# Kernel optimization log

Measured on AMD Instinct MI355X. Metric: run time of the kernel, lower is better.

## Reference

```python
import jax, jax.numpy as jnp
import numpy as np

EMB = 1024
HEAD = 64  # emb_size // head_nb = 1024 // 16

def setup_inputs() -> dict:
    key = jax.random.key(0)
    kx, kq, kk, kv = jax.random.split(key, 4)
    x = jax.random.normal(kx, (8, 2048, EMB), dtype=jnp.float32)
    # torch nn.Linear(EMB, HEAD) weight has shape [HEAD, EMB]; y = x @ W.T
    s = 1.0 / np.sqrt(EMB)
    Wq = jax.random.uniform(kq, (HEAD, EMB), jnp.float32, -s, s)
    Wk = jax.random.uniform(kk, (HEAD, EMB), jnp.float32, -s, s)
    Wv = jax.random.uniform(kv, (HEAD, EMB), jnp.float32, -s, s)
    return {"x": x, "Wq": Wq, "Wk": Wk, "Wv": Wv}

def reference(x, Wq, Wk, Wv):
    B, T, C = x.shape
    q = jnp.einsum('btc,hc->bth', x, Wq)  # [B,T,H]
    k = jnp.einsum('btc,hc->bth', x, Wk)
    v = jnp.einsum('btc,hc->bth', x, Wv)
    scale = 1.0 / jnp.sqrt(jnp.float32(q.shape[-1]))
    wei = jnp.einsum('bth,bsh->bts', q, k) * scale  # [B,T,T]
    causal = jnp.tril(jnp.ones((T, T), dtype=bool))
    wei = jnp.where(causal, wei, -jnp.inf)
    wei = jax.nn.softmax(wei, axis=-1)
    # dropout is identity in eval mode
    out = jnp.einsum('bts,bsh->bth', wei, v)  # [B,T,H]
    return out
```

## Files before the change

### kernel.cpp

```cpp
#include <hip/hip_runtime.h>
#include <math.h>

#define SEQ  2048
#define NROW 16384
#define HEAD 64
#define EMB  1024

typedef __attribute__((ext_vector_type(8))) short short8;
typedef __attribute__((ext_vector_type(4))) float f32x4;

static __device__ __forceinline__ unsigned short f2bf(float f) {
    unsigned u = __builtin_bit_cast(unsigned, f);
    u += 0x7fffu + ((u >> 16) & 1u);
    return (unsigned short)(u >> 16);
}
static __device__ __forceinline__ float bf2f(unsigned short u) {
    unsigned v = (unsigned)u << 16;
    return __builtin_bit_cast(float, v);
}
static __device__ __forceinline__ ushort4 cvt4(float4 f) {
    ushort4 u;
    u.x = f2bf(f.x); u.y = f2bf(f.y); u.z = f2bf(f.z); u.w = f2bf(f.w);
    return u;
}

static __device__ __forceinline__ void gload_lds16(const void* g, void* l) {
    __builtin_amdgcn_global_load_lds(
        (const __attribute__((address_space(1))) unsigned int*)g,
        (__attribute__((address_space(3))) unsigned int*)l, 16, 0, 0);
}

__global__ __launch_bounds__(256) void wcvt_kernel(
    const float* __restrict__ Wq, const float* __restrict__ Wk,
    const float* __restrict__ Wv, unsigned short* __restrict__ Wb)
{
    const int idx = (blockIdx.x * 256 + threadIdx.x) * 4;
    const int h = idx >> 10;
    const float* src;
    if (h < 64)       src = Wq + idx;
    else if (h < 128) src = Wk + (idx - 65536);
    else              src = Wv + (idx - 131072);
    *(ushort4*)(Wb + idx) = cvt4(*(const float4*)src);
}

__global__ __launch_bounds__(512, 2) void qkv_mfma_kernel(
    const float* __restrict__ x, const unsigned short* __restrict__ Wb,
    unsigned short* __restrict__ qN, unsigned short* __restrict__ kN,
    unsigned short* __restrict__ vT)
{
    __shared__ unsigned short As[2][64][72];
    __shared__ unsigned short Bs[2][192 * 64];

    const int tid  = threadIdx.x;
    const int w    = tid >> 6;
    const int lane = tid & 63;
    const int col  = lane & 15;
    const int quad = lane >> 4;
    const int row0 = blockIdx.x * 64;
    const int wm   = w >> 2;
    const int wn   = w & 3;
    const int pq   = (quad ^ (col & 7)) * 8;

    const int ar_r = tid >> 4, ar_c = tid & 15;
    const float* xg = x + (size_t)(row0 + ar_r) * EMB + ar_c * 4;

    const int sr = lane >> 3, cc = (lane & 7) ^ sr;
    const unsigned short* bg = Wb;

    {
        float4 fa[2];
#pragma unroll
        for (int j = 0; j < 2; ++j) fa[j] = *(const float4*)(xg + (size_t)(32 * j) * EMB);
#pragma unroll
        for (int j = 0; j < 2; ++j) *(ushort4*)&As[0][ar_r + 32 * j][ar_c * 4] = cvt4(fa[j]);
#pragma unroll
        for (int j = 0; j < 3; ++j) {
            const int c = w * 3 + j;
            gload_lds16(bg + (size_t)(c * 8 + sr) * EMB + cc * 8,
                        &Bs[0][c * 8 * 64]);
        }
    }
    __syncthreads();

    f32x4 acc[2][3];
#pragma unroll
    for (int mf = 0; mf < 2; ++mf)
#pragma unroll
        for (int t = 0; t < 3; ++t) acc[mf][t] = (f32x4){0.f, 0.f, 0.f, 0.f};

    float4 fa[2];
#pragma unroll 2
    for (int kt = 0; kt < 16; ++kt) {
        const int cur = kt & 1;
        if (kt + 1 < 16) {
            const int k0 = (kt + 1) * 64;
#pragma unroll
            for (int j = 0; j < 3; ++j) {
                const int c = w * 3 + j;
                gload_lds16(bg + (size_t)(c * 8 + sr) * EMB + k0 + cc * 8,
                            &Bs[cur ^ 1][c * 8 * 64]);
            }
#pragma unroll
            for (int j = 0; j < 2; ++j)
                fa[j] = *(const float4*)(xg + (size_t)(32 * j) * EMB + k0);
        }
#pragma unroll
        for (int ks = 0; ks < 2; ++ks) {
            short8 af0 = *(const short8*)&As[cur][wm * 32 + col][ks * 32 + quad * 8];
            short8 af1 = *(const short8*)&As[cur][wm * 32 + 16 + col][ks * 32 + quad * 8];
            const int po = pq ^ (ks * 32);
#pragma unroll
            for (int t = 0; t < 3; ++t) {
                short8 bf = *(const short8*)
                    &Bs[cur][(wn * 48 + t * 16 + col) * 64 + po];
                acc[0][t] = __builtin_amdgcn_mfma_f32_16x16x32_bf16(af0, bf, acc[0][t], 0, 0, 0);
                acc[1][t] = __builtin_amdgcn_mfma_f32_16x16x32_bf16(af1, bf, acc[1][t], 0, 0, 0);
            }
        }
        if (kt + 1 < 16) {
#pragma unroll
            for (int j = 0; j < 2; ++j)
                *(ushort4*)&As[cur ^ 1][ar_r + 32 * j][ar_c * 4] = cvt4(fa[j]);
        }
        __syncthreads();
    }

#pragma unroll
    for (int mf = 0; mf < 2; ++mf) {
        const int ro = row0 + wm * 32 + mf * 16 + quad * 4;
#pragma unroll
        for (int t = 0; t < 3; ++t) {
            const int hb = wn * 48 + 16 * t;
            const int h  = hb + col;
            if (hb < 64) {
#pragma unroll
                for (int r = 0; r < 4; ++r)
                    qN[(size_t)(ro + r) * HEAD + h] = f2bf(acc[mf][t][r] * 0.125f);
            } else if (hb < 128) {
#pragma unroll
                for (int r = 0; r < 4; ++r)
                    kN[(size_t)(ro + r) * HEAD + (h - 64)] = f2bf(acc[mf][t][r]);
            } else {
                ushort4 uv;
                uv.x = f2bf(acc[mf][t][0]); uv.y = f2bf(acc[mf][t][1]);
                uv.z = f2bf(acc[mf][t][2]); uv.w = f2bf(acc[mf][t][3]);
                *(ushort4*)(vT + (size_t)(h - 128) * NROW + ro) = uv;
            }
        }
    }
}

__global__ __launch_bounds__(512, 2) void attn_kernel(
    const unsigned short* __restrict__ qN,
    const unsigned short* __restrict__ kN,
    const unsigned short* __restrict__ vT,
    unsigned short* __restrict__ op,
    float2* __restrict__ ml)
{
    __shared__ unsigned short Ks[2][64 * 64];
    __shared__ unsigned short Vs[2][64 * 64];
    __shared__ unsigned short Pl[8][32][72];

    const int qt   = 7 - (int)blockIdx.x;
    const int b    = blockIdx.y;
    const int p    = blockIdx.z;
    const int tid  = threadIdx.x;
    const int wv   = tid >> 6;
    const int lane = tid & 63;
    const int col  = lane & 15;
    const int quad = lane >> 4;

    const int q0   = qt * 256 + wv * 16;
    const int q0g  = b * SEQ + q0;
    const int Cb   = 4 * qt + 4;
    const int kt0  = (Cb * p) >> 2;
    const int kt1  = (Cb * (p + 1)) >> 2;
    const int ktp  = min(kt0, Cb - 1);

    const int sr = lane >> 3, cc = (lane & 7) ^ sr;
    const int pq = (quad ^ (col & 7)) * 8;
    const unsigned short* kgb = kN + (size_t)(b * SEQ) * HEAD;
    const int bcol = b * SEQ;

    const short8* qp0 = (const short8*)qN + (size_t)(q0g + col) * 8;
    const short8* qp1 = (const short8*)qN + (size_t)(q0g + 128 + col) * 8;
    short8 aq00 = qp0[quad], aq01 = qp0[quad + 4];
    short8 aq10 = qp1[quad], aq11 = qp1[quad + 4];

    f32x4 o[2][4];
    float l_i[2][4];
#pragma unroll
    for (int mi = 0; mi < 2; ++mi)
#pragma unroll
        for (int t = 0; t < 4; ++t) {
            o[mi][t] = (f32x4){0.f, 0.f, 0.f, 0.f};
            l_i[mi][t] = 0.f;
        }

    {
        const int r = wv * 8 + sr;
        gload_lds16(kgb + (size_t)(ktp * 64 + r) * HEAD + cc * 8,
                    &Ks[0][wv * 8 * 64]);
        gload_lds16(vT + (size_t)r * NROW + bcol + ktp * 64 + cc * 8,
                    &Vs[0][wv * 8 * 64]);
    }
    __syncthreads();

    for (int kt = kt0; kt < kt1; ++kt) {
        const int cur = (kt - kt0) & 1;
        const int s0  = kt * 64;
        const bool dz = (kt >= Cb - 4);
        const bool m0 = (kt < Cb - 2);

        if (kt + 1 < kt1) {
            const int r = wv * 8 + sr;
            gload_lds16(kgb + (size_t)((kt + 1) * 64 + r) * HEAD + cc * 8,
                        &Ks[cur ^ 1][wv * 8 * 64]);
            gload_lds16(vT + (size_t)r * NROW + bcol + (kt + 1) * 64 + cc * 8,
                        &Vs[cur ^ 1][wv * 8 * 64]);
        }

        f32x4 sv[2][4];
#pragma unroll
        for (int t = 0; t < 4; ++t) {
            sv[0][t] = (f32x4){0.f, 0.f, 0.f, 0.f};
            sv[1][t] = (f32x4){0.f, 0.f, 0.f, 0.f};
        }
#pragma unroll
        for (int t = 0; t < 4; ++t) {
            const int rb = (16 * t + col) * 64;
            short8 kf0 = *(const short8*)&Ks[cur][rb + pq];
            short8 kf1 = *(const short8*)&Ks[cur][rb + (pq ^ 32)];
            sv[1][t] = __builtin_amdgcn_mfma_f32_16x16x32_bf16(aq10, kf0, sv[1][t], 0, 0, 0);
            sv[1][t] = __builtin_amdgcn_mfma_f32_16x16x32_bf16(aq11, kf1, sv[1][t], 0, 0, 0);
            if (m0) {
                sv[0][t] = __builtin_amdgcn_mfma_f32_16x16x32_bf16(aq00, kf0, sv[0][t], 0, 0, 0);
                sv[0][t] = __builtin_amdgcn_mfma_f32_16x16x32_bf16(aq01, kf1, sv[0][t], 0, 0, 0);
            }
        }

#pragma unroll
        for (int mi = 0; mi < 2; ++mi) {
            if (mi == 0 && !m0) continue;
#pragma unroll
            for (int r = 0; r < 4; ++r) {
                const int grow = q0 + mi * 128 + quad * 4 + r;
                float ls = 0.f;
#pragma unroll
                for (int t = 0; t < 4; ++t) {
                    float e = __expf(sv[mi][t][r]);
                    if (dz && (s0 + 16 * t + col > grow)) e = 0.0f;
                    Pl[wv][mi * 16 + quad * 4 + r][16 * t + col] = f2bf(e);
                    ls += e;
                }
                l_i[mi][r] += ls;
            }
        }

        short8 pf00, pf01;
        if (m0) {
            pf00 = *(const short8*)&Pl[wv][col][quad * 8];
            pf01 = *(const short8*)&Pl[wv][col][quad * 8 + 32];
        }
        short8 pf10 = *(const short8*)&Pl[wv][16 + col][quad * 8];
        short8 pf11 = *(const short8*)&Pl[wv][16 + col][quad * 8 + 32];

#pragma unroll
        for (int tn = 0; tn < 4; ++tn) {
            const int rb = (16 * tn + col) * 64;
            short8 vf0 = *(const short8*)&Vs[cur][rb + pq];
            short8 vf1 = *(const short8*)&Vs[cur][rb + (pq ^ 32)];
            o[1][tn] = __builtin_amdgcn_mfma_f32_16x16x32_bf16(pf10, vf0, o[1][tn], 0, 0, 0);
            o[1][tn] = __builtin_amdgcn_mfma_f32_16x16x32_bf16(pf11, vf1, o[1][tn], 0, 0, 0);
            if (m0) {
                o[0][tn] = __builtin_amdgcn_mfma_f32_16x16x32_bf16(pf00, vf0, o[0][tn], 0, 0, 0);
                o[0][tn] = __builtin_amdgcn_mfma_f32_16x16x32_bf16(pf01, vf1, o[0][tn], 0, 0, 0);
            }
        }

        __syncthreads();
    }

#pragma unroll
    for (int mi = 0; mi < 2; ++mi) {
#pragma unroll
        for (int r = 0; r < 4; ++r) {
            float l = l_i[mi][r];
            l += __shfl_xor(l, 1, 16);
            l += __shfl_xor(l, 2, 16);
            l += __shfl_xor(l, 4, 16);
            l += __shfl_xor(l, 8, 16);
            l_i[mi][r] = l;
        }
        const int ro = q0g + mi * 128 + quad * 4;
#pragma unroll
        for (int tn = 0; tn < 4; ++tn)
#pragma unroll
            for (int r = 0; r < 4; ++r)
                op[((size_t)p * NROW + ro + r) * HEAD + 16 * tn + col] =
                    f2bf(o[mi][tn][r]);
        if (col == 0) {
#pragma unroll
            for (int r = 0; r < 4; ++r)
                ml[p * NROW + ro + r] = make_float2(0.0f, l_i[mi][r]);
        }
    }
}

__global__ __launch_bounds__(256) void merge_kernel(
    const unsigned short* __restrict__ op, const float2* __restrict__ ml,
    float* __restrict__ out)
{
    const int idx = blockIdx.x * 256 + threadIdx.x;
    const int row = idx >> 4;
    const int hc  = (idx & 15) * 4;

    float denom = 0.0f;
#pragma unroll
    for (int p = 0; p < 4; ++p) denom += ml[p * NROW + row].y;
    const float inv = 1.0f / denom;

    float4 r = make_float4(0.f, 0.f, 0.f, 0.f);
#pragma unroll
    for (int p = 0; p < 4; ++p) {
        ushort4 u = *(const ushort4*)(op + ((size_t)p * NROW + row) * HEAD + hc);
        r.x += bf2f(u.x);
        r.y += bf2f(u.y);
        r.z += bf2f(u.z);
        r.w += bf2f(u.w);
    }
    r.x *= inv; r.y *= inv; r.z *= inv; r.w *= inv;
    *(float4*)(out + (size_t)row * HEAD + hc) = r;
}

extern "C" void kernel_launch(void* const* d_in, const int* in_sizes, int n_in,
                              void* d_out, int out_size, void* d_ws, size_t ws_size,
                              hipStream_t stream)
{
    const float* x  = (const float*)d_in[0];
    const float* Wq = (const float*)d_in[1];
    const float* Wk = (const float*)d_in[2];
    const float* Wv = (const float*)d_in[3];

    char* w = (char*)d_ws;
    unsigned short* qN = (unsigned short*)w;
    unsigned short* kN = (unsigned short*)(w + (2u << 20));
    unsigned short* vT = (unsigned short*)(w + (4u << 20));
    unsigned short* Wb = (unsigned short*)(w + (6u << 20));
    unsigned short* op = (unsigned short*)(w + (6u << 20) + 393216);
    float2*         ml = (float2*)(w + (14u << 20) + 393216);
    float* out = (float*)d_out;

    wcvt_kernel<<<192, 256, 0, stream>>>(Wq, Wk, Wv, Wb);
    qkv_mfma_kernel<<<256, 512, 0, stream>>>(x, Wb, qN, kN, vT);
    attn_kernel<<<dim3(8, 8, 4), 512, 0, stream>>>(qN, kN, vT, op, ml);
    merge_kernel<<<1024, 256, 0, stream>>>(op, ml, out);
}
```

Measured before the change: 138.1 us.

## Fuse four kernels into one cooperative kernel with grid-wide syncs

Merges the weight conversion, QKV projection GEMM, causal attention and split merge into one persistent cooperative kernel of 256 blocks. Stages are separated by grid.sync() with thread fences rather than by separate launches. This is meant to remove three kernel-launch gaps and the drain and fill between kernels. In exchange it drops the occupancy hint in launch bounds, depends on all 256 blocks of 512 threads being co-resident, and adds grid barrier cost plus load imbalance in the attention stage.

Measured after the change: 380.4 us. +175.5%, slower.

```diff
diff --git a/kernel.cpp b/kernel.cpp
--- a/kernel.cpp
+++ b/kernel.cpp
@@ -1,5 +1,8 @@
 #include <hip/hip_runtime.h>
+#include <hip/hip_cooperative_groups.h>
 #include <math.h>
+
+namespace cg = cooperative_groups;
 
 #define SEQ  2048
 #define NROW 16384
@@ -30,307 +33,318 @@
         (__attribute__((address_space(3))) unsigned int*)l, 16, 0, 0);
 }
 
-__global__ __launch_bounds__(256) void wcvt_kernel(
-    const float* __restrict__ Wq, const float* __restrict__ Wk,
-    const float* __restrict__ Wv, unsigned short* __restrict__ Wb)
+__global__ __launch_bounds__(512) void fused_kernel(
+    const float* __restrict__ x, const float* __restrict__ Wq,
+    const float* __restrict__ Wk, const float* __restrict__ Wv,
+    unsigned short* __restrict__ Wb, unsigned short* __restrict__ qN,
+    unsigned short* __restrict__ kN, unsigned short* __restrict__ vT,
+    unsigned short* __restrict__ op,
+    float2* __restrict__ ml,
+    float* __restrict__ out)
 {
-    const int idx = (blockIdx.x * 256 + threadIdx.x) * 4;
-    const int h = idx >> 10;
-    const float* src;
-    if (h < 64)       src = Wq + idx;
-    else if (h < 128) src = Wk + (idx - 65536);
-    else              src = Wv + (idx - 131072);
-    *(ushort4*)(Wb + idx) = cvt4(*(const float4*)src);
-}
-
-__global__ __launch_bounds__(512, 2) void qkv_mfma_kernel(
-    const float* __restrict__ x, const unsigned short* __restrict__ Wb,
-    unsigned short* __restrict__ qN, unsigned short* __restrict__ kN,
-    unsigned short* __restrict__ vT)
-{
-    __shared__ unsigned short As[2][64][72];
-    __shared__ unsigned short Bs[2][192 * 64];
-
-    const int tid  = threadIdx.x;
-    const int w    = tid >> 6;
-    const int lane = tid & 63;
-    const int col  = lane & 15;
-    const int quad = lane >> 4;
-    const int row0 = blockIdx.x * 64;
-    const int wm   = w >> 2;
-    const int wn   = w & 3;
-    const int pq   = (quad ^ (col & 7)) * 8;
-
-    const int ar_r = tid >> 4, ar_c = tid & 15;
-    const float* xg = x + (size_t)(row0 + ar_r) * EMB + ar_c * 4;
-
-    const int sr = lane >> 3, cc = (lane & 7) ^ sr;
-    const unsigned short* bg = Wb;
+    __shared__ __align__(16) char smem[69632];
+    cg::grid_group grid = cg::this_grid();
+
+    const int tid = threadIdx.x;
+    const int bid = blockIdx.x;
 
     {
-        float4 fa[2];
-#pragma unroll
-        for (int j = 0; j < 2; ++j) fa[j] = *(const float4*)(xg + (size_t)(32 * j) * EMB);
-#pragma unroll
-        for (int j = 0; j < 2; ++j) *(ushort4*)&As[0][ar_r + 32 * j][ar_c * 4] = cvt4(fa[j]);
-#pragma unroll
-        for (int j = 0; j < 3; ++j) {
-            const int c = w * 3 + j;
-            gload_lds16(bg + (size_t)(c * 8 + sr) * EMB + cc * 8,
-                        &Bs[0][c * 8 * 64]);
+        const int gid = bid * 512 + tid;
+        if (gid < 49152) {
+            const int idx = gid * 4;
+            const int h = idx >> 10;
+            const float* src;
+            if (h < 64)       src = Wq + idx;
+            else if (h < 128) src = Wk + (idx - 65536);
+            else              src = Wv + (idx - 131072);
+            *(ushort4*)(Wb + idx) = cvt4(*(const float4*)src);
         }
     }
-    __syncthreads();
-
-    f32x4 acc[2][3];
-#pragma unroll
-    for (int mf = 0; mf < 2; ++mf)
-#pragma unroll
-        for (int t = 0; t < 3; ++t) acc[mf][t] = (f32x4){0.f, 0.f, 0.f, 0.f};
-
-    float4 fa[2];
-#pragma unroll 2
-    for (int kt = 0; kt < 16; ++kt) {
-        const int cur = kt & 1;
-        if (kt + 1 < 16) {
-            const int k0 = (kt + 1) * 64;
+    __threadfence();
+    grid.sync();
+
+    {
+        unsigned short (*As)[64][72] = (unsigned short (*)[64][72])smem;
+        unsigned short (*Bs)[192 * 64] =
+            (unsigned short (*)[192 * 64])(smem + 18432);
+
+        const int w    = tid >> 6;
+        const int lane = tid & 63;
+        const int col  = lane & 15;
+        const int quad = lane >> 4;
+        const int row0 = bid * 64;
+        const int wm   = w >> 2;
+        const int wn   = w & 3;
+        const int pq   = (quad ^ (col & 7)) * 8;
+
+        const int ar_r = tid >> 4, ar_c = tid & 15;
+        const float* xg = x + (size_t)(row0 + ar_r) * EMB + ar_c * 4;
+
+        const int sr = lane >> 3, cc = (lane & 7) ^ sr;
+        const unsigned short* bg = Wb;
+
+        {
+            float4 fa[2];
+#pragma unroll
+            for (int j = 0; j < 2; ++j) fa[j] = *(const float4*)(xg + (size_t)(32 * j) * EMB);
+#pragma unroll
+            for (int j = 0; j < 2; ++j) *(ushort4*)&As[0][ar_r + 32 * j][ar_c * 4] = cvt4(fa[j]);
 #pragma unroll
             for (int j = 0; j < 3; ++j) {
                 const int c = w * 3 + j;
-                gload_lds16(bg + (size_t)(c * 8 + sr) * EMB + k0 + cc * 8,
-                            &Bs[cur ^ 1][c * 8 * 64]);
-            }
-#pragma unroll
-            for (int j = 0; j < 2; ++j)
-                fa[j] = *(const float4*)(xg + (size_t)(32 * j) * EMB + k0);
-        }
-#pragma unroll
-        for (int ks = 0; ks < 2; ++ks) {
-            short8 af0 = *(const short8*)&As[cur][wm * 32 + col][ks * 32 + quad * 8];
-            short8 af1 = *(const short8*)&As[cur][wm * 32 + 16 + col][ks * 32 + quad * 8];
-            const int po = pq ^ (ks * 32);
+                gload_lds16(bg + (size_t)(c * 8 + sr) * EMB + cc * 8,
+                            &Bs[0][c * 8 * 64]);
+            }
+        }
+        __syncthreads();
+
+        f32x4 acc[2][3];
+#pragma unroll
+        for (int mf = 0; mf < 2; ++mf)
+#pragma unroll
+            for (int t = 0; t < 3; ++t) acc[mf][t] = (f32x4){0.f, 0.f, 0.f, 0.f};
+
+        float4 fa[2];
+#pragma unroll 2
+        for (int kt = 0; kt < 16; ++kt) {
+            const int cur = kt & 1;
+            if (kt + 1 < 16) {
+                const int k0 = (kt + 1) * 64;
+#pragma unroll
+                for (int j = 0; j < 3; ++j) {
+                    const int c = w * 3 + j;
+                    gload_lds16(bg + (size_t)(c * 8 + sr) * EMB + k0 + cc * 8,
+                                &Bs[cur ^ 1][c * 8 * 64]);
+                }
+#pragma unroll
+                for (int j = 0; j < 2; ++j)
+                    fa[j] = *(const float4*)(xg + (size_t)(32 * j) * EMB + k0);
+            }
+#pragma unroll
+            for (int ks = 0; ks < 2; ++ks) {
+                short8 af0 = *(const short8*)&As[cur][wm * 32 + col][ks * 32 + quad * 8];
+                short8 af1 = *(const short8*)&As[cur][wm * 32 + 16 + col][ks * 32 + quad * 8];
+                const int po = pq ^ (ks * 32);
+#pragma unroll
+                for (int t = 0; t < 3; ++t) {
+                    short8 bf = *(const short8*)
+                        &Bs[cur][(wn * 48 + t * 16 + col) * 64 + po];
+                    acc[0][t] = __builtin_amdgcn_mfma_f32_16x16x32_bf16(af0, bf, acc[0][t], 0, 0, 0);
+                    acc[1][t] = __builtin_amdgcn_mfma_f32_16x16x32_bf16(af1, bf, acc[1][t], 0, 0, 0);
+                }
+            }
+            if (kt + 1 < 16) {
+#pragma unroll
+                for (int j = 0; j < 2; ++j)
+                    *(ushort4*)&As[cur ^ 1][ar_r + 32 * j][ar_c * 4] = cvt4(fa[j]);
+            }
+            __syncthreads();
+        }
+
+#pragma unroll
+        for (int mf = 0; mf < 2; ++mf) {
+            const int ro = row0 + wm * 32 + mf * 16 + quad * 4;
 #pragma unroll
             for (int t = 0; t < 3; ++t) {
-                short8 bf = *(const short8*)
-                    &Bs[cur][(wn * 48 + t * 16 + col) * 64 + po];
-                acc[0][t] = __builtin_amdgcn_mfma_f32_16x16x32_bf16(af0, bf, acc[0][t], 0, 0, 0);
-                acc[1][t] = __builtin_amdgcn_mfma_f32_16x16x32_bf16(af1, bf, acc[1][t], 0, 0, 0);
-            }
-        }
-        if (kt + 1 < 16) {
-#pragma unroll
-            for (int j = 0; j < 2; ++j)
-                *(ushort4*)&As[cur ^ 1][ar_r + 32 * j][ar_c * 4] = cvt4(fa[j]);
+                const int hb = wn * 48 + 16 * t;
+                const int h  = hb + col;
+                if (hb < 64) {
+#pragma unroll
+                    for (int r = 0; r < 4; ++r)
+                        qN[(size_t)(ro + r) * HEAD + h] = f2bf(acc[mf][t][r] * 0.125f);
+                } else if (hb < 128) {
+#pragma unroll
+                    for (int r = 0; r < 4; ++r)
+                        kN[(size_t)(ro + r) * HEAD + (h - 64)] = f2bf(acc[mf][t][r]);
+                } else {
+                    ushort4 uv;
+                    uv.x = f2bf(acc[mf][t][0]); uv.y = f2bf(acc[mf][t][1]);
+                    uv.z = f2bf(acc[mf][t][2]); uv.w = f2bf(acc[mf][t][3]);
+                    *(ushort4*)(vT + (size_t)(h - 128) * NROW + ro) = uv;
+                }
+            }
+        }
+    }
+    __threadfence();
+    grid.sync();
+
+    {
+        unsigned short (*Ks)[64 * 64] = (unsigned short (*)[64 * 64])smem;
+        unsigned short (*Vs)[64 * 64] = (unsigned short (*)[64 * 64])(smem + 16384);
+        unsigned short (*Pl)[32][72]  = (unsigned short (*)[32][72])(smem + 32768);
+
+        const int qt   = 7 - (bid & 7);
+        const int b    = (bid >> 3) & 7;
+        const int p    = bid >> 6;
+        const int wv   = tid >> 6;
+        const int lane = tid & 63;
+        const int col  = lane & 15;
+        const int quad = lane >> 4;
+
+        const int q0   = qt * 256 + wv * 16;
+        const int q0g  = b * SEQ + q0;
+        const int Cb   = 4 * qt + 4;
+        const int kt0  = (Cb * p) >> 2;
+        const int kt1  = (Cb * (p + 1)) >> 2;
+        const int ktp  = min(kt0, Cb - 1);
+
+        const int sr = lane >> 3, cc = (lane & 7) ^ sr;
+        const int pq = (quad ^ (col & 7)) * 8;
+        const unsigned short* kgb = kN + (size_t)(b * SEQ) * HEAD;
+        const int bcol = b * SEQ;
+
+        const short8* qp0 = (const short8*)qN + (size_t)(q0g + col) * 8;
+        const short8* qp1 = (const short8*)qN + (size_t)(q0g + 128 + col) * 8;
+        short8 aq00 = qp0[quad], aq01 = qp0[quad + 4];
+        short8 aq10 = qp1[quad], aq11 = qp1[quad + 4];
+
+        f32x4 o[2][4];
+        float l_i[2][4];
+#pragma unroll
+        for (int mi = 0; mi < 2; ++mi)
+#pragma unroll
+            for (int t = 0; t < 4; ++t) {
+                o[mi][t] = (f32x4){0.f, 0.f, 0.f, 0.f};
+                l_i[mi][t] = 0.f;
+            }
+
+        {
+            const int r = wv * 8 + sr;
+            gload_lds16(kgb + (size_t)(ktp * 64 + r) * HEAD + cc * 8,
+                        &Ks[0][wv * 8 * 64]);
+            gload_lds16(vT + (size_t)r * NROW + bcol + ktp * 64 + cc * 8,
+                        &Vs[0][wv * 8 * 64]);
         }
         __syncthreads();
+
+        for (int kt = kt0; kt < kt1; ++kt) {
+            const int cur = (kt - kt0) & 1;
+            const int s0  = kt * 64;
+            const bool dz = (kt >= Cb - 4);
+            const bool m0 = (kt < Cb - 2);
+
+            if (kt + 1 < kt1) {
+                const int r = wv * 8 + sr;
+                gload_lds16(kgb + (size_t)((kt + 1) * 64 + r) * HEAD + cc * 8,
+                            &Ks[cur ^ 1][wv * 8 * 64]);
+                gload_lds16(vT + (size_t)r * NROW + bcol + (kt + 1) * 64 + cc * 8,
+                            &Vs[cur ^ 1][wv * 8 * 64]);
+            }
+
+            f32x4 sv[2][4];
+#pragma unroll
+            for (int t = 0; t < 4; ++t) {
+                sv[0][t] = (f32x4){0.f, 0.f, 0.f, 0.f};
+                sv[1][t] = (f32x4){0.f, 0.f, 0.f, 0.f};
+            }
+#pragma unroll
+            for (int t = 0; t < 4; ++t) {
+                const int rb = (16 * t + col) * 64;
+                short8 kf0 = *(const short8*)&Ks[cur][rb + pq];
+                short8 kf1 = *(const short8*)&Ks[cur][rb + (pq ^ 32)];
+                sv[1][t] = __builtin_amdgcn_mfma_f32_16x16x32_bf16(aq10, kf0, sv[1][t], 0, 0, 0);
+                sv[1][t] = __builtin_amdgcn_mfma_f32_16x16x32_bf16(aq11, kf1, sv[1][t], 0, 0, 0);
+                if (m0) {
+                    sv[0][t] = __builtin_amdgcn_mfma_f32_16x16x32_bf16(aq00, kf0, sv[0][t], 0, 0, 0);
+                    sv[0][t] = __builtin_amdgcn_mfma_f32_16x16x32_bf16(aq01, kf1, sv[0][t], 0, 0, 0);
+                }
+            }
+
+#pragma unroll
+            for (int mi = 0; mi < 2; ++mi) {
+                if (mi == 0 && !m0) continue;
+#pragma unroll
+                for (int r = 0; r < 4; ++r) {
+                    const int grow = q0 + mi * 128 + quad * 4 + r;
+                    float ls = 0.f;
+#pragma unroll
+                    for (int t = 0; t < 4; ++t) {
+                        float e = __expf(sv[mi][t][r]);
+                        if (dz && (s0 + 16 * t + col > grow)) e = 0.0f;
+                        Pl[wv][mi * 16 + quad * 4 + r][16 * t + col] = f2bf(e);
+                        ls += e;
+                    }
+                    l_i[mi][r] += ls;
+                }
+            }
+
+            short8 pf00, pf01;
+            if (m0) {
+                pf00 = *(const short8*)&Pl[wv][col][quad * 8];
+                pf01 = *(const short8*)&Pl[wv][col][quad * 8 + 32];
+            }
+            short8 pf10 = *(const short8*)&Pl[wv][16 + col][quad * 8];
+            short8 pf11 = *(const short8*)&Pl[wv][16 + col][quad * 8 + 32];
+
+#pragma unroll
+            for (int tn = 0; tn < 4; ++tn) {
+                const int rb = (16 * tn + col) * 64;
+                short8 vf0 = *(const short8*)&Vs[cur][rb + pq];
+                short8 vf1 = *(const short8*)&Vs[cur][rb + (pq ^ 32)];
+                o[1][tn] = __builtin_amdgcn_mfma_f32_16x16x32_bf16(pf10, vf0, o[1][tn], 0, 0, 0);
+                o[1][tn] = __builtin_amdgcn_mfma_f32_16x16x32_bf16(pf11, vf1, o[1][tn], 0, 0, 0);
+                if (m0) {
+                    o[0][tn] = __builtin_amdgcn_mfma_f32_16x16x32_bf16(pf00, vf0, o[0][tn], 0, 0, 0);
+                    o[0][tn] = __builtin_amdgcn_mfma_f32_16x16x32_bf16(pf01, vf1, o[0][tn], 0, 0, 0);
+                }
+            }
+
+            __syncthreads();
+        }
+
+#pragma unroll
+        for (int mi = 0; mi < 2; ++mi) {
+#pragma unroll
+            for (int r = 0; r < 4; ++r) {
+                float l = l_i[mi][r];
+                l += __shfl_xor(l, 1, 16);
+                l += __shfl_xor(l, 2, 16);
+                l += __shfl_xor(l, 4, 16);
+                l += __shfl_xor(l, 8, 16);
+                l_i[mi][r] = l;
+            }
+            const int ro = q0g + mi * 128 + quad * 4;
+#pragma unroll
+            for (int tn = 0; tn < 4; ++tn)
+#pragma unroll
+                for (int r = 0; r < 4; ++r)
+                    op[((size_t)p * NROW + ro + r) * HEAD + 16 * tn + col] =
+                        f2bf(o[mi][tn][r]);
+            if (col == 0) {
+#pragma unroll
+                for (int r = 0; r < 4; ++r)
+                    ml[p * NROW + ro + r] = make_float2(0.0f, l_i[mi][r]);
+            }
+        }
     }
-
-#pragma unroll
-    for (int mf = 0; mf < 2; ++mf) {
-        const int ro = row0 + wm * 32 + mf * 16 + quad * 4;
-#pragma unroll
-        for (int t = 0; t < 3; ++t) {
-            const int hb = wn * 48 + 16 * t;
-            const int h  = hb + col;
-            if (hb < 64) {
-#pragma unroll
-                for (int r = 0; r < 4; ++r)
-                    qN[(size_t)(ro + r) * HEAD + h] = f2bf(acc[mf][t][r] * 0.125f);
-            } else if (hb < 128) {
-#pragma unroll
-                for (int r = 0; r < 4; ++r)
-                    kN[(size_t)(ro + r) * HEAD + (h - 64)] = f2bf(acc[mf][t][r]);
-            } else {
-                ushort4 uv;
-                uv.x = f2bf(acc[mf][t][0]); uv.y = f2bf(acc[mf][t][1]);
-                uv.z = f2bf(acc[mf][t][2]); uv.w = f2bf(acc[mf][t][3]);
-                *(ushort4*)(vT + (size_t)(h - 128) * NROW + ro) = uv;
-            }
+    __threadfence();
+    grid.sync();
+
+    {
+#pragma unroll
+        for (int ii = 0; ii < 2; ++ii) {
+            const int idx = ii * 131072 + bid * 512 + tid;
+            const int row = idx >> 4;
+            const int hc  = (idx & 15) * 4;
+
+            float denom = 0.0f;
+#pragma unroll
+            for (int p = 0; p < 4; ++p) denom += ml[p * NROW + row].y;
+            const float inv = 1.0f / denom;
+
+            float4 r = make_float4(0.f, 0.f, 0.f, 0.f);
+#pragma unroll
+            for (int p = 0; p < 4; ++p) {
+                ushort4 u = *(const ushort4*)(op + ((size_t)p * NROW + row) * HEAD + hc);
+                r.x += bf2f(u.x);
+                r.y += bf2f(u.y);
+                r.z += bf2f(u.z);
+                r.w += bf2f(u.w);
+            }
+            r.x *= inv; r.y *= inv; r.z *= inv; r.w *= inv;
+            *(float4*)(out + (size_t)row * HEAD + hc) = r;
         }
     }
-}
-
-__global__ __launch_bounds__(512, 2) void attn_kernel(
-    const unsigned short* __restrict__ qN,
-    const unsigned short* __restrict__ kN,
-    const unsigned short* __restrict__ vT,
-    unsigned short* __restrict__ op,
-    float2* __restrict__ ml)
-{
-    __shared__ unsigned short Ks[2][64 * 64];
-    __shared__ unsigned short Vs[2][64 * 64];
-    __shared__ unsigned short Pl[8][32][72];
-
-    const int qt   = 7 - (int)blockIdx.x;
-    const int b    = blockIdx.y;
-    const int p    = blockIdx.z;
-    const int tid  = threadIdx.x;
-    const int wv   = tid >> 6;
-    const int lane = tid & 63;
-    const int col  = lane & 15;
-    const int quad = lane >> 4;
-
-    const int q0   = qt * 256 + wv * 16;
-    const int q0g  = b * SEQ + q0;
-    const int Cb   = 4 * qt + 4;
-    const int kt0  = (Cb * p) >> 2;
-    const int kt1  = (Cb * (p + 1)) >> 2;
-    const int ktp  = min(kt0, Cb - 1);
-
-    const int sr = lane >> 3, cc = (lane & 7) ^ sr;
-    const int pq = (quad ^ (col & 7)) * 8;
-    const unsigned short* kgb = kN + (size_t)(b * SEQ) * HEAD;
-    const int bcol = b * SEQ;
-
-    const short8* qp0 = (const short8*)qN + (size_t)(q0g + col) * 8;
-    const short8* qp1 = (const short8*)qN + (size_t)(q0g + 128 + col) * 8;
-    short8 aq00 = qp0[quad], aq01 = qp0[quad + 4];
-    short8 aq10 = qp1[quad], aq11 = qp1[quad + 4];
-
-    f32x4 o[2][4];
-    float l_i[2][4];
-#pragma unroll
-    for (int mi = 0; mi < 2; ++mi)
-#pragma unroll
-        for (int t = 0; t < 4; ++t) {
-            o[mi][t] = (f32x4){0.f, 0.f, 0.f, 0.f};
-            l_i[mi][t] = 0.f;
-        }
-
-    {
-        const int r = wv * 8 + sr;
-        gload_lds16(kgb + (size_t)(ktp * 64 + r) * HEAD + cc * 8,
-                    &Ks[0][wv * 8 * 64]);
-        gload_lds16(vT + (size_t)r * NROW + bcol + ktp * 64 + cc * 8,
-                    &Vs[0][wv * 8 * 64]);
-    }
-    __syncthreads();
-
-    for (int kt = kt0; kt < kt1; ++kt) {
-        const int cur = (kt - kt0) & 1;
-        const int s0  = kt * 64;
-        const bool dz = (kt >= Cb - 4);
-        const bool m0 = (kt < Cb - 2);
-
-        if (kt + 1 < kt1) {
-            const int r = wv * 8 + sr;
-            gload_lds16(kgb + (size_t)((kt + 1) * 64 + r) * HEAD + cc * 8,
-                        &Ks[cur ^ 1][wv * 8 * 64]);
-            gload_lds16(vT + (size_t)r * NROW + bcol + (kt + 1) * 64 + cc * 8,
-                        &Vs[cur ^ 1][wv * 8 * 64]);
-        }
-
-        f32x4 sv[2][4];
-#pragma unroll
-        for (int t = 0; t < 4; ++t) {
-            sv[0][t] = (f32x4){0.f, 0.f, 0.f, 0.f};
-            sv[1][t] = (f32x4){0.f, 0.f, 0.f, 0.f};
-        }
-#pragma unroll
-        for (int t = 0; t < 4; ++t) {
-            const int rb = (16 * t + col) * 64;
-            short8 kf0 = *(const short8*)&Ks[cur][rb + pq];
-            short8 kf1 = *(const short8*)&Ks[cur][rb + (pq ^ 32)];
-            sv[1][t] = __builtin_amdgcn_mfma_f32_16x16x32_bf16(aq10, kf0, sv[1][t], 0, 0, 0);
-            sv[1][t] = __builtin_amdgcn_mfma_f32_16x16x32_bf16(aq11, kf1, sv[1][t], 0, 0, 0);
-            if (m0) {
-                sv[0][t] = __builtin_amdgcn_mfma_f32_16x16x32_bf16(aq00, kf0, sv[0][t], 0, 0, 0);
-                sv[0][t] = __builtin_amdgcn_mfma_f32_16x16x32_bf16(aq01, kf1, sv[0][t], 0, 0, 0);
-            }
-        }
-
-#pragma unroll
-        for (int mi = 0; mi < 2; ++mi) {
-            if (mi == 0 && !m0) continue;
-#pragma unroll
-            for (int r = 0; r < 4; ++r) {
-                const int grow = q0 + mi * 128 + quad * 4 + r;
-                float ls = 0.f;
-#pragma unroll
-                for (int t = 0; t < 4; ++t) {
-                    float e = __expf(sv[mi][t][r]);
-                    if (dz && (s0 + 16 * t + col > grow)) e = 0.0f;
-                    Pl[wv][mi * 16 + quad * 4 + r][16 * t + col] = f2bf(e);
-                    ls += e;
-                }
-                l_i[mi][r] += ls;
-            }
-        }
-
-        short8 pf00, pf01;
-        if (m0) {
-            pf00 = *(const short8*)&Pl[wv][col][quad * 8];
-            pf01 = *(const short8*)&Pl[wv][col][quad * 8 + 32];
-        }
-        short8 pf10 = *(const short8*)&Pl[wv][16 + col][quad * 8];
-        short8 pf11 = *(const short8*)&Pl[wv][16 + col][quad * 8 + 32];
-
-#pragma unroll
-        for (int tn = 0; tn < 4; ++tn) {
-            const int rb = (16 * tn + col) * 64;
-            short8 vf0 = *(const short8*)&Vs[cur][rb + pq];
-            short8 vf1 = *(const short8*)&Vs[cur][rb + (pq ^ 32)];
-            o[1][tn] = __builtin_amdgcn_mfma_f32_16x16x32_bf16(pf10, vf0, o[1][tn], 0, 0, 0);
-            o[1][tn] = __builtin_amdgcn_mfma_f32_16x16x32_bf16(pf11, vf1, o[1][tn], 0, 0, 0);
-            if (m0) {
-                o[0][tn] = __builtin_amdgcn_mfma_f32_16x16x32_bf16(pf00, vf0, o[0][tn], 0, 0, 0);
-                o[0][tn] = __builtin_amdgcn_mfma_f32_16x16x32_bf16(pf01, vf1, o[0][tn], 0, 0, 0);
-            }
-        }
-
-        __syncthreads();
-    }
-
-#pragma unroll
-    for (int mi = 0; mi < 2; ++mi) {
-#pragma unroll
-        for (int r = 0; r < 4; ++r) {
-            float l = l_i[mi][r];
-            l += __shfl_xor(l, 1, 16);
-            l += __shfl_xor(l, 2, 16);
-            l += __shfl_xor(l, 4, 16);
-            l += __shfl_xor(l, 8, 16);
-            l_i[mi][r] = l;
-        }
-        const int ro = q0g + mi * 128 + quad * 4;
-#pragma unroll
-        for (int tn = 0; tn < 4; ++tn)
-#pragma unroll
-            for (int r = 0; r < 4; ++r)
-                op[((size_t)p * NROW + ro + r) * HEAD + 16 * tn + col] =
-                    f2bf(o[mi][tn][r]);
-        if (col == 0) {
-#pragma unroll
-            for (int r = 0; r < 4; ++r)
-                ml[p * NROW + ro + r] = make_float2(0.0f, l_i[mi][r]);
-        }
-    }
-}
-
-__global__ __launch_bounds__(256) void merge_kernel(
-    const unsigned short* __restrict__ op, const float2* __restrict__ ml,
-    float* __restrict__ out)
-{
-    const int idx = blockIdx.x * 256 + threadIdx.x;
-    const int row = idx >> 4;
-    const int hc  = (idx & 15) * 4;
-
-    float denom = 0.0f;
-#pragma unroll
-    for (int p = 0; p < 4; ++p) denom += ml[p * NROW + row].y;
-    const float inv = 1.0f / denom;
-
-    float4 r = make_float4(0.f, 0.f, 0.f, 0.f);
-#pragma unroll
-    for (int p = 0; p < 4; ++p) {
-        ushort4 u = *(const ushort4*)(op + ((size_t)p * NROW + row) * HEAD + hc);
-        r.x += bf2f(u.x);
-        r.y += bf2f(u.y);
-        r.z += bf2f(u.z);
-        r.w += bf2f(u.w);
-    }
-    r.x *= inv; r.y *= inv; r.z *= inv; r.w *= inv;
-    *(float4*)(out + (size_t)row * HEAD + hc) = r;
 }
 
 extern "C" void kernel_launch(void* const* d_in, const int* in_sizes, int n_in,
@@ -351,8 +365,7 @@
     float2*         ml = (float2*)(w + (14u << 20) + 393216);
     float* out = (float*)d_out;
 
-    wcvt_kernel<<<192, 256, 0, stream>>>(Wq, Wk, Wv, Wb);
-    qkv_mfma_kernel<<<256, 512, 0, stream>>>(x, Wb, qN, kN, vT);
-    attn_kernel<<<dim3(8, 8, 4), 512, 0, stream>>>(qN, kN, vT, op, ml);
-    merge_kernel<<<1024, 256, 0, stream>>>(op, ml, out);
-}
+    void* args[] = {&x, &Wq, &Wk, &Wv, &Wb, &qN, &kN, &vT, &op, &ml, &out};
+    hipLaunchCooperativeKernel((void*)fused_kernel, dim3(256), dim3(512),
+                               args, 0, stream);
+}
```
